# Kernel optimization log

Hardware: AMD Instinct MI355X
Metric: run time of the kernel (lower is better)

The kernel has to match this reference:

```python
import jax, jax.numpy as jnp
import numpy as np

THETA = 100000.0

def _rope(x, pos, theta=THETA):
    # x: [..., H, S, d_k]; pos: [S] int
    d_k = x.shape[-1]
    half = d_k // 2
    inv_freq = theta ** (-(jnp.arange(half, dtype=jnp.float32) / half))  # theta^{-2i/d}
    ang = pos.astype(jnp.float32)[:, None] * inv_freq[None, :]  # [S, half]
    cos, sin = jnp.cos(ang), jnp.sin(ang)
    x1 = x[..., 0::2]
    x2 = x[..., 1::2]
    r1 = x1 * cos - x2 * sin
    r2 = x1 * sin + x2 * cos
    # interleave back to [..., d_k]
    return jnp.stack([r1, r2], axis=-1).reshape(x.shape)


def setup_inputs() -> dict:
    key = jax.random.key(0)
    ks = jax.random.split(key, 5)
    B, S, D = 1, 4096, 1024
    x = jax.random.normal(ks[0], (B, S, D), dtype=jnp.float32)
    sc = 1.0 / np.sqrt(D)
    Wq = jax.random.normal(ks[1], (D, D), dtype=jnp.float32) * sc
    Wk = jax.random.normal(ks[2], (D, D), dtype=jnp.float32) * sc
    Wv = jax.random.normal(ks[3], (D, D), dtype=jnp.float32) * sc
    Wo = jax.random.normal(ks[4], (D, D), dtype=jnp.float32) * sc
    token_positions = jnp.arange(S, dtype=jnp.int32)
    return {"x": x, "Wq": Wq, "Wk": Wk, "Wv": Wv, "Wo": Wo, "token_positions": token_positions}


def reference(x, Wq, Wk, Wv, Wo, token_positions):
    H = 16
    B, S, D = x.shape
    d_k = D // H
    # Linear (no bias): y = x @ W^T
    Q = jnp.einsum('bsd,ed->bse', x, Wq)
    K = jnp.einsum('bsd,ed->bse', x, Wk)
    V = jnp.einsum('bsd,ed->bse', x, Wv)
    # [B, H, S, d_k]
    Q = Q.reshape(B, S, H, d_k).transpose(0, 2, 1, 3)
    K = K.reshape(B, S, H, d_k).transpose(0, 2, 1, 3)
    V = V.reshape(B, S, H, d_k).transpose(0, 2, 1, 3)
    Q = _rope(Q, token_positions)
    K = _rope(K, token_positions)
    scores = jnp.einsum('bhqd,bhkd->bhqk', Q, K) / jnp.sqrt(jnp.float32(d_k))
    causal = jnp.tril(jnp.ones((S, S), dtype=bool))
    scores = jnp.where(causal, scores, jnp.finfo(scores.dtype).min)
    probs = jax.nn.softmax(scores, axis=-1)
    attn = jnp.einsum('bhqk,bhkd->bhqd', probs, V)
    attn = attn.transpose(0, 2, 1, 3).reshape(B, S, D)
    return jnp.einsum('bsd,ed->bse', attn, Wo)
```

## Files before the change

### kernel.cpp

```cpp
#include <hip/hip_runtime.h>

typedef float f32x4 __attribute__((ext_vector_type(4)));
typedef short s16x8 __attribute__((ext_vector_type(8)));
typedef int   i32x2 __attribute__((ext_vector_type(2)));
typedef int   i32x4 __attribute__((ext_vector_type(4)));

#define DEV static __device__ __forceinline__

DEV short f2bf(float f) {
    unsigned u = __builtin_bit_cast(unsigned, f);
    u += 0x7FFFu + ((u >> 16) & 1u);
    return (short)(u >> 16);
}
DEV float bf2f(short s) {
    return __builtin_bit_cast(float, ((unsigned)(unsigned short)s) << 16);
}
DEV int cvtpk(float lo, float hi) {
    int r;
    asm("v_cvt_pk_bf16_f32 %0, %1, %2" : "=v"(r) : "v"(lo), "v"(hi));
    return r;
}
DEV float fexp2(float x) { float r; asm("v_exp_f32 %0, %1" : "=v"(r) : "v"(x)); return r; }
DEV float ffract(float x){ float r; asm("v_fract_f32 %0, %1" : "=v"(r) : "v"(x)); return r; }
DEV float fsin(float x)  { float r; asm("v_sin_f32 %0, %1" : "=v"(r) : "v"(x)); return r; }
DEV float fcos(float x)  { float r; asm("v_cos_f32 %0, %1" : "=v"(r) : "v"(x)); return r; }
DEV f32x4 mfma_bf16(s16x8 a, s16x8 b, f32x4 c) {
    asm("v_mfma_f32_16x16x32_bf16 %0, %1, %2, %0" : "+v"(c) : "v"(a), "v"(b));
    return c;
}
DEV f32x4 mfma16_bf16(i32x2 a, i32x2 b, f32x4 c) {
    asm("v_mfma_f32_16x16x16_bf16 %0, %1, %2, %0" : "+v"(c) : "v"(a), "v"(b));
    return c;
}
DEV void gl_lds16(const void* g, void* l) {
    __builtin_amdgcn_global_load_lds((const __attribute__((address_space(1))) unsigned*)g,
                                     (__attribute__((address_space(3))) unsigned*)l, 16, 0, 0);
}

__global__ __launch_bounds__(256) void conv_kernel(
    const float* __restrict__ x,
    const float* __restrict__ W0, const float* __restrict__ W1,
    const float* __restrict__ W2, const float* __restrict__ W3,
    short* __restrict__ xb,
    short* __restrict__ B0, short* __restrict__ B1,
    short* __restrict__ B2, short* __restrict__ B3)
{
    const int bid = blockIdx.x, tid = threadIdx.x;
    const float* src;
    short* dst;
    size_t off;
    if (bid < 2048) {
        src = x; dst = xb; off = (size_t)bid * 2048 + tid * 8;
    } else {
        int t = bid - 2048, wi = t >> 9;
        src = wi == 0 ? W0 : (wi == 1 ? W1 : (wi == 2 ? W2 : W3));
        dst = wi == 0 ? B0 : (wi == 1 ? B1 : (wi == 2 ? B2 : B3));
        off = (size_t)(t & 511) * 2048 + tid * 8;
    }
    f32x4 v0 = *(const f32x4*)(src + off);
    f32x4 v1 = *(const f32x4*)(src + off + 4);
    s16x8 o;
    #pragma unroll
    for (int e = 0; e < 4; e++) { o[e] = f2bf(v0[e]); o[4 + e] = f2bf(v1[e]); }
    *(s16x8*)(dst + off) = o;
}

template<int BM, int OUT_BF16, int ROPE>
__global__ __launch_bounds__(256) void gemm128(
    const short* __restrict__ A,
    const short* __restrict__ Bq, const short* __restrict__ Bk, const short* __restrict__ Bv,
    void* __restrict__ Cq, void* __restrict__ Ck, void* __restrict__ Cv,
    const int* __restrict__ posp)
{
    constexpr int KD = 1024, ND = 1024;
    constexpr int MI = BM / 32;
    __shared__ __align__(16) short As[BM * 32];
    __shared__ __align__(16) short Bs[128 * 32];
    const int n0 = blockIdx.x * 128, m0 = blockIdx.y * BM;
    const int zz = blockIdx.z;
    const short* B = zz == 0 ? Bq : (zz == 1 ? Bk : Bv);
    void* C       = zz == 0 ? Cq : (zz == 1 ? Ck : Cv);
    const int tid = threadIdx.x;
    const int lane = tid & 63, w = tid >> 6, g = lane >> 4, c = lane & 15;
    const int wm = w >> 1, wn = w & 1;

    const int swz = (tid & 3) ^ ((tid >> 3) & 3);
    const short* a0 = A + (size_t)(m0 + (tid >> 2)) * KD + 8 * swz;
    const short* a1 = a0 + (size_t)64 * KD;
    const short* b0 = B + (size_t)(n0 + (tid >> 2)) * KD + 8 * swz;
    const short* b1 = b0 + (size_t)64 * KD;
    char* ldsA = (char*)As + w * 1024;
    char* ldsB = (char*)Bs + w * 1024;

    int aoff[MI], boff[4];
    #pragma unroll
    for (int i = 0; i < MI; i++) {
        int ar = wm * (BM / 2) + i * 16 + c;
        aoff[i] = ar * 64 + (g ^ ((ar >> 1) & 3)) * 16;
    }
    #pragma unroll
    for (int j = 0; j < 4; j++) {
        int br = wn * 64 + j * 16 + c;
        boff[j] = br * 64 + (g ^ ((br >> 1) & 3)) * 16;
    }

    f32x4 acc[MI][4] = {};

    for (int k0 = 0; k0 < KD; k0 += 32) {
        __syncthreads();
        gl_lds16(a0 + k0, ldsA);
        if (BM == 128) gl_lds16(a1 + k0, ldsA + 4096);
        gl_lds16(b0 + k0, ldsB);
        gl_lds16(b1 + k0, ldsB + 4096);
        __syncthreads();
        s16x8 af[MI], bf[4];
        #pragma unroll
        for (int i = 0; i < MI; i++) af[i] = *(const s16x8*)((const char*)As + aoff[i]);
        #pragma unroll
        for (int j = 0; j < 4; j++) bf[j] = *(const s16x8*)((const char*)Bs + boff[j]);
        #pragma unroll
        for (int i = 0; i < MI; i++)
            #pragma unroll
            for (int j = 0; j < 4; j++)
                acc[i][j] = mfma_bf16(af[i], bf[j], acc[i][j]);
    }

    if (ROPE && zz <= 1) {
        const float ps = (zz == 0) ? 0.18033688011112042f : 1.0f;
        #pragma unroll
        for (int j = 0; j < 4; j++) {
            int col = n0 + wn * 64 + j * 16 + c;
            float invf = fexp2(-(float)((col & 63) >> 1) * 0.51905126482615036f)
                       * 0.15915494309189535f;
            float ssign = (col & 1) ? 1.f : -1.f;
            #pragma unroll
            for (int i = 0; i < MI; i++)
                #pragma unroll
                for (int r = 0; r < 4; r++) {
                    int row = m0 + wm * (BM / 2) + i * 16 + 4 * g + r;
                    float fp = (float)posp[row];
                    float fr = ffract(fp * invf);
                    float sn = fsin(fr) * ps, cs = fcos(fr) * ps;
                    float own = acc[i][j][r];
                    float oth = __shfl_xor(own, 1);
                    acc[i][j][r] = own * cs + oth * (ssign * sn);
                }
        }
    }

    #pragma unroll
    for (int i = 0; i < MI; i++)
        #pragma unroll
        for (int j = 0; j < 4; j++)
            #pragma unroll
            for (int r = 0; r < 4; r++) {
                int row = m0 + wm * (BM / 2) + i * 16 + 4 * g + r;
                int col = n0 + wn * 64 + j * 16 + c;
                float v = acc[i][j][r];
                if (OUT_BF16) ((short*)C)[(size_t)row * ND + col] = f2bf(v);
                else          ((float*)C)[(size_t)row * ND + col] = v;
            }
}

template<int A_BF16, int OUT_BF16>
__global__ __launch_bounds__(256) void gemm_bt(
    const void* __restrict__ Ap,
    const float* __restrict__ B0, const float* __restrict__ B1, const float* __restrict__ B2,
    void* __restrict__ C0, void* __restrict__ C1, void* __restrict__ C2)
{
    constexpr int KD = 1024, ND = 1024;
    __shared__ short As[64][40];
    __shared__ short Bs[64][40];
    const int n0 = blockIdx.x * 64, m0 = blockIdx.y * 64;
    const float* Bw = blockIdx.z == 0 ? B0 : (blockIdx.z == 1 ? B1 : B2);
    void* Cw       = blockIdx.z == 0 ? C0 : (blockIdx.z == 1 ? C1 : C2);
    const int tid = threadIdx.x;
    const int lane = tid & 63, w = tid >> 6, g = lane >> 4, c = lane & 15;
    const int wm = w >> 1, wn = w & 1;
    const int sr = tid >> 2, scc = (tid & 3) * 8;

    f32x4 acc[2][2] = {};

    for (int k0 = 0; k0 < KD; k0 += 32) {
        __syncthreads();
        if (A_BF16) {
            *(s16x8*)&As[sr][scc] =
                *(const s16x8*)((const short*)Ap + (size_t)(m0 + sr) * KD + k0 + scc);
        } else {
            const float* ap = (const float*)Ap + (size_t)(m0 + sr) * KD + k0 + scc;
            f32x4 va = *(const f32x4*)ap, vb = *(const f32x4*)(ap + 4);
            s16x8 av;
            #pragma unroll
            for (int e = 0; e < 4; e++) { av[e] = f2bf(va[e]); av[4 + e] = f2bf(vb[e]); }
            *(s16x8*)&As[sr][scc] = av;
        }
        {
            const float* bp = Bw + (size_t)(n0 + sr) * KD + k0 + scc;
            f32x4 va = *(const f32x4*)bp, vb = *(const f32x4*)(bp + 4);
            s16x8 bv;
            #pragma unroll
            for (int e = 0; e < 4; e++) { bv[e] = f2bf(va[e]); bv[4 + e] = f2bf(vb[e]); }
            *(s16x8*)&Bs[sr][scc] = bv;
        }
        __syncthreads();
        s16x8 af[2], bfv[2];
        #pragma unroll
        for (int i = 0; i < 2; i++) af[i]  = *(const s16x8*)&As[wm * 32 + i * 16 + c][8 * g];
        #pragma unroll
        for (int j = 0; j < 2; j++) bfv[j] = *(const s16x8*)&Bs[wn * 32 + j * 16 + c][8 * g];
        #pragma unroll
        for (int i = 0; i < 2; i++)
            #pragma unroll
            for (int j = 0; j < 2; j++)
                acc[i][j] = mfma_bf16(af[i], bfv[j], acc[i][j]);
    }

    #pragma unroll
    for (int i = 0; i < 2; i++)
        #pragma unroll
        for (int j = 0; j < 2; j++)
            #pragma unroll
            for (int r = 0; r < 4; r++) {
                int row = m0 + wm * 32 + i * 16 + 4 * g + r;
                int col = n0 + wn * 32 + j * 16 + c;
                float v = acc[i][j][r];
                if (OUT_BF16) ((short*)Cw)[(size_t)row * ND + col] = f2bf(v);
                else          ((float*)Cw)[(size_t)row * ND + col] = v;
            }
}

__global__ __launch_bounds__(256) void rope_kernel(short* Q, short* K, const int* __restrict__ posp)
{
    const int t = blockIdx.x * 256 + threadIdx.x;
    const int isK = blockIdx.y;
    short* ptr = isK ? K : Q;
    const float postscale = isK ? 1.0f : 0.18033688011112042f;
    const int idx  = t * 8;
    const int srow = idx >> 10;
    const int dd   = (idx & 1023) & 63;
    const int p0   = dd >> 1;
    const float fp = (float)posp[srow];
    s16x8 v = *(s16x8*)(ptr + idx);
    s16x8 o;
    #pragma unroll
    for (int pr = 0; pr < 4; pr++) {
        float ex  = fexp2(-(float)(p0 + pr) * 0.51905126482615036f);
        float ang = fp * ex * 0.15915494309189535f;
        float fr  = ffract(ang);
        float sn  = fsin(fr) * postscale;
        float cs  = fcos(fr) * postscale;
        float x1 = bf2f(v[2 * pr]), x2 = bf2f(v[2 * pr + 1]);
        o[2 * pr]     = f2bf(x1 * cs - x2 * sn);
        o[2 * pr + 1] = f2bf(x1 * sn + x2 * cs);
    }
    *(s16x8*)(ptr + idx) = o;
}

template<int SPLIT>
__global__ __launch_bounds__(512, 2) void attn_kernel(
    const short* __restrict__ Q, const short* __restrict__ K,
    const short* __restrict__ V, short* __restrict__ O0,
    short* __restrict__ O1, float* __restrict__ Lf)
{
    constexpr int D = 1024;
    constexpr int ST = 1 + SPLIT;
    int qx, h, z;
    if (SPLIT) {
        const int B = blockIdx.x;
        const int xcd = B & 7, k = B >> 3;
        h = xcd + 8 * (k >> 5);
        const int r = k & 31;
        qx = r & 15;
        z = r >> 4;
    } else {
        qx = blockIdx.x; h = blockIdx.y; z = 0;
    }
    const int hc = h * 64;
    short* O = (SPLIT && z) ? O1 : O0;
    const int tid = threadIdx.x;
    const int w = tid >> 6, lane = tid & 63, g = lane >> 4, c = lane & 15;

    __shared__ __align__(16) int Kl[2][64 * 32];
    __shared__ __align__(16) int Vl[2][64][32];

    const int wk = w & 3;
    const int krow_l = lane >> 3;
    const int kchunk = (lane & 7) ^ krow_l;
    const short* Kpre = K + hc + (size_t)(wk * 16 + krow_l) * D + kchunk * 8;
    char* kdst0 = (char*)&Kl[0][0] + wk * 16 * 128;
    char* kdst1 = (char*)&Kl[1][0] + wk * 16 * 128;

    const int vtid = tid & 255;
    const int vkvp = vtid & 31;
    const int vd0 = (vtid >> 5) * 8;
    const short* Vpre = V + hc + (size_t)(2 * vkvp) * D + vd0;

    int koff0[4], koff1[4];
    #pragma unroll
    for (int t = 0; t < 4; t++) {
        int row = t * 16 + c;
        koff0[t] = row * 128 + ((g) ^ (row & 7)) * 16;
        koff1[t] = row * 128 + ((4 + g) ^ (row & 7)) * 16;
    }

    for (int pi = 0; pi < 2; pi++) {
        const int qq = pi ? 31 - qx : qx;
        const int wq_min = qq * 128 + w * 16;
        const int qrow = wq_min + c;
        const short* qp = Q + (size_t)qrow * D + hc + 8 * g;
        const s16x8 bq0 = *(const s16x8*)qp;
        const s16x8 bq1 = *(const s16x8*)(qp + 32);

        f32x4 acc[4] = {};
        float l = 0.f;
        const int nkb = 2 * qq + 2;

        __syncthreads();
        s16x8 vs0, vs1;
        {
            if (w < 4) {
                gl_lds16(Kpre + (size_t)(z * 64) * D, kdst0);
                gl_lds16(Kpre + (size_t)(z * 64 + 8) * D, kdst0 + 8 * 128);
            } else {
                const short* vp = Vpre + (size_t)(z * 64) * D;
                vs0 = *(const s16x8*)vp;
                vs1 = *(const s16x8*)(vp + D);
            }
        }

        int cur = 0;
        for (int kb = z; kb < nkb; kb += ST, cur ^= 1) {
            if (w >= 4) {
                #pragma unroll
                for (int e = 0; e < 8; e++) {
                    unsigned dw = (unsigned)(unsigned short)vs0[e] | ((unsigned)(unsigned short)vs1[e] << 16);
                    Vl[cur][vd0 + e][vkvp ^ (4 * e)] = (int)dw;
                }
            }
            asm volatile("s_waitcnt vmcnt(0)" ::: "memory");
            __syncthreads();

            const bool more = (kb + ST) < nkb;
            if (more) {
                const int kb1 = kb + ST;
                if (w < 4) {
                    char* kd = cur ? kdst0 : kdst1;
                    gl_lds16(Kpre + (size_t)(kb1 * 64) * D, kd);
                    gl_lds16(Kpre + (size_t)(kb1 * 64 + 8) * D, kd + 8 * 128);
                } else {
                    const short* vp = Vpre + (size_t)(kb1 * 64) * D;
                    vs0 = *(const s16x8*)vp;
                    vs1 = *(const s16x8*)(vp + D);
                }
            }

            if (kb * 64 > wq_min + 15) continue;

            const char* Kb = (const char*)&Kl[cur][0];
            f32x4 st[4];
            __builtin_amdgcn_s_setprio(1);
            #pragma unroll
            for (int t = 0; t < 4; t++) {
                s16x8 a0 = *(const s16x8*)(Kb + koff0[t]);
                s16x8 a1 = *(const s16x8*)(Kb + koff1[t]);
                f32x4 zf = {};
                zf = mfma_bf16(a0, bq0, zf);
                zf = mfma_bf16(a1, bq1, zf);
                st[t] = zf;
            }
            __builtin_amdgcn_s_setprio(0);

            float p[16];
            if (kb * 64 + 63 > wq_min) {
                #pragma unroll
                for (int t = 0; t < 4; t++)
                    #pragma unroll
                    for (int i = 0; i < 4; i++) {
                        int kv = kb * 64 + t * 16 + 4 * g + i;
                        float e = fexp2(st[t][i]);
                        if (kv > qrow) e = 0.f;
                        p[t * 4 + i] = e;
                        l += e;
                    }
            } else {
                #pragma unroll
                for (int t = 0; t < 4; t++)
                    #pragma unroll
                    for (int i = 0; i < 4; i++) {
                        float e = fexp2(st[t][i]);
                        p[t * 4 + i] = e;
                        l += e;
                    }
            }

            i32x2 pd[4];
            #pragma unroll
            for (int t = 0; t < 4; t++) {
                pd[t][0] = cvtpk(p[t * 4 + 0], p[t * 4 + 1]);
                pd[t][1] = cvtpk(p[t * 4 + 2], p[t * 4 + 3]);
            }

            __builtin_amdgcn_s_setprio(1);
            #pragma unroll
            for (int t = 0; t < 4; t++) {
                #pragma unroll
                for (int jt = 0; jt < 4; jt++) {
                    i32x2 vb = *(const i32x2*)&Vl[cur][jt * 16 + c][(t * 8 + 2 * g) ^ (4 * (c & 7))];
                    acc[jt] = mfma16_bf16(pd[t], vb, acc[jt]);
                }
            }
            __builtin_amdgcn_s_setprio(0);
        }

        float lsum = l + __shfl_xor(l, 16);
        lsum += __shfl_xor(lsum, 32);
        if (SPLIT && lane < 16) {
            float Lv = (lsum > 0.f) ? __log2f(lsum) : -1e30f;
            Lf[(size_t)(z * 16 + h) * 4096 + (qq * 128 + w * 16 + lane)] = Lv;
        }
        float linv[4];
        #pragma unroll
        for (int i = 0; i < 4; i++) {
            float ls = __shfl(lsum, 4 * g + i);
            linv[i] = (ls > 0.f) ? 1.f / ls : 0.f;
        }
        #pragma unroll
        for (int jt = 0; jt < 4; jt++)
            #pragma unroll
            for (int i = 0; i < 4; i++) {
                int r = qq * 128 + w * 16 + 4 * g + i;
                O[(size_t)r * D + hc + jt * 16 + c] = f2bf(acc[jt][i] * linv[i]);
            }
    }
}

__global__ __launch_bounds__(256) void combine_kernel(
    short* __restrict__ Aw, const short* __restrict__ P1, const float* __restrict__ Lf)
{
    const int t = blockIdx.x * 256 + threadIdx.x;
    const int idx = t * 8;
    const int row = idx >> 10, col = idx & 1023, h = col >> 6;
    float L0 = Lf[(size_t)h * 4096 + row];
    float L1 = Lf[(size_t)(16 + h) * 4096 + row];
    float LM = fmaxf(L0, L1);
    float w0 = fexp2(L0 - LM), w1 = fexp2(L1 - LM);
    float inv = 1.f / (w0 + w1);
    w0 *= inv; w1 *= inv;
    s16x8 a = *(s16x8*)(Aw + idx);
    s16x8 b = *(const s16x8*)(P1 + idx);
    s16x8 o;
    #pragma unroll
    for (int e = 0; e < 8; e++)
        o[e] = f2bf(w0 * bf2f(a[e]) + w1 * bf2f(b[e]));
    *(s16x8*)(Aw + idx) = o;
}

extern "C" void kernel_launch(void* const* d_in, const int* in_sizes, int n_in,
                              void* d_out, int out_size, void* d_ws, size_t ws_size,
                              hipStream_t stream)
{
    const float* x  = (const float*)d_in[0];
    const float* Wq = (const float*)d_in[1];
    const float* Wk = (const float*)d_in[2];
    const float* Wv = (const float*)d_in[3];
    const float* Wo = (const float*)d_in[4];
    const int*  pos = (const int*)d_in[5];
    float* out = (float*)d_out;

    const size_t SD = (size_t)4096 * 1024;
    const size_t WSZ = (size_t)1024 * 1024;
    short* Qw = (short*)d_ws;
    short* Kw = Qw + SD;
    short* Vw = Kw + SD;
    short* Aw = Vw + SD;

    const size_t need_A = (5 * SD + 4 * WSZ) * sizeof(short) + 2 * 16 * 4096 * sizeof(float);
    const size_t need_B = (4 * SD + 4 * WSZ) * sizeof(short);

    if (ws_size >= need_A) {
        short* P1  = Aw + SD;
        short* xb  = Aw;
        short* Wqb = P1 + SD;
        short* Wkb = Wqb + WSZ;
        short* Wvb = Wkb + WSZ;
        short* Wob = Wvb + WSZ;
        float* Lf  = (float*)(Wob + WSZ);
        conv_kernel<<<4096, 256, 0, stream>>>(x, Wq, Wk, Wv, Wo, xb, Wqb, Wkb, Wvb, Wob);
        gemm128<128, 1, 1><<<dim3(8, 32, 3), 256, 0, stream>>>(xb, Wqb, Wkb, Wvb, Qw, Kw, Vw, pos);
        attn_kernel<1><<<512, 512, 0, stream>>>(Qw, Kw, Vw, Aw, P1, Lf);
        combine_kernel<<<2048, 256, 0, stream>>>(Aw, P1, Lf);
        gemm128<64, 0, 0><<<dim3(8, 64, 1), 256, 0, stream>>>(Aw, Wob, Wob, Wob, out, out, out, pos);
    } else if (ws_size >= need_B) {
        short* xb  = Aw;
        short* Wqb = Aw + SD;
        short* Wkb = Wqb + WSZ;
        short* Wvb = Wkb + WSZ;
        short* Wob = Wvb + WSZ;
        conv_kernel<<<4096, 256, 0, stream>>>(x, Wq, Wk, Wv, Wo, xb, Wqb, Wkb, Wvb, Wob);
        gemm128<128, 1, 1><<<dim3(8, 32, 3), 256, 0, stream>>>(xb, Wqb, Wkb, Wvb, Qw, Kw, Vw, pos);
        attn_kernel<0><<<dim3(16, 16, 1), 512, 0, stream>>>(Qw, Kw, Vw, Aw, Aw, nullptr);
        gemm128<64, 0, 0><<<dim3(8, 64, 1), 256, 0, stream>>>(Aw, Wob, Wob, Wob, out, out, out, pos);
    } else {
        gemm_bt<0, 1><<<dim3(16, 64, 3), 256, 0, stream>>>(x, Wq, Wk, Wv, Qw, Kw, Vw);
        rope_kernel<<<dim3(2048, 2), 256, 0, stream>>>(Qw, Kw, pos);
        attn_kernel<0><<<dim3(16, 16, 1), 512, 0, stream>>>(Qw, Kw, Vw, Aw, Aw, nullptr);
        gemm_bt<1, 0><<<dim3(16, 64, 1), 256, 0, stream>>>(Aw, Wo, Wo, Wo, out, out, out);
    }
}
```

Before: 131.2 us.

## Split attention KV range four ways with generalized log-sum-exp combine

Generalizes the split-KV attention kernel from two to NZ partitions and launches a 4-way split (1024 blocks) when the workspace is large enough. The combine kernel merges NP partial outputs using per-row log2 sums. The aim is more parallelism to fill CUs and balance the causal workload. In exchange, it adds extra partial-output writes and reads, and raises the launch bound occupancy hint, which may force register limits or spills.

```diff
diff --git a/kernel.cpp b/kernel.cpp
--- a/kernel.cpp
+++ b/kernel.cpp
@@ -256,27 +256,27 @@
     *(s16x8*)(ptr + idx) = o;
 }
 
-template<int SPLIT>
-__global__ __launch_bounds__(512, 2) void attn_kernel(
+template<int NZ>
+__global__ __launch_bounds__(512, 8) void attn_kernel(
     const short* __restrict__ Q, const short* __restrict__ K,
     const short* __restrict__ V, short* __restrict__ O0,
-    short* __restrict__ O1, float* __restrict__ Lf)
+    short* __restrict__ O1, short* __restrict__ O2, short* __restrict__ O3,
+    float* __restrict__ Lf)
 {
     constexpr int D = 1024;
-    constexpr int ST = 1 + SPLIT;
     int qx, h, z;
-    if (SPLIT) {
+    if (NZ > 1) {
         const int B = blockIdx.x;
         const int xcd = B & 7, k = B >> 3;
-        h = xcd + 8 * (k >> 5);
-        const int r = k & 31;
+        h = xcd + 8 * (k / (16 * NZ));
+        const int r = k % (16 * NZ);
         qx = r & 15;
         z = r >> 4;
     } else {
         qx = blockIdx.x; h = blockIdx.y; z = 0;
     }
     const int hc = h * 64;
-    short* O = (SPLIT && z) ? O1 : O0;
+    short* O = (z == 0) ? O0 : (z == 1 ? O1 : (z == 2 ? O2 : O3));
     const int tid = threadIdx.x;
     const int w = tid >> 6, lane = tid & 63, g = lane >> 4, c = lane & 15;
 
@@ -329,7 +329,7 @@
         }
 
         int cur = 0;
-        for (int kb = z; kb < nkb; kb += ST, cur ^= 1) {
+        for (int kb = z; kb < nkb; kb += NZ, cur ^= 1) {
             if (w >= 4) {
                 #pragma unroll
                 for (int e = 0; e < 8; e++) {
@@ -340,9 +340,9 @@
             asm volatile("s_waitcnt vmcnt(0)" ::: "memory");
             __syncthreads();
 
-            const bool more = (kb + ST) < nkb;
+            const bool more = (kb + NZ) < nkb;
             if (more) {
-                const int kb1 = kb + ST;
+                const int kb1 = kb + NZ;
                 if (w < 4) {
                     char* kd = cur ? kdst0 : kdst1;
                     gl_lds16(Kpre + (size_t)(kb1 * 64) * D, kd);
@@ -414,7 +414,7 @@
 
         float lsum = l + __shfl_xor(l, 16);
         lsum += __shfl_xor(lsum, 32);
-        if (SPLIT && lane < 16) {
+        if (NZ > 1 && lane < 16) {
             float Lv = (lsum > 0.f) ? __log2f(lsum) : -1e30f;
             Lf[(size_t)(z * 16 + h) * 4096 + (qq * 128 + w * 16 + lane)] = Lv;
         }
@@ -434,24 +434,42 @@
     }
 }
 
+template<int NP>
 __global__ __launch_bounds__(256) void combine_kernel(
-    short* __restrict__ Aw, const short* __restrict__ P1, const float* __restrict__ Lf)
+    short* __restrict__ Aw, const short* __restrict__ P1,
+    const short* __restrict__ P2, const short* __restrict__ P3,
+    const float* __restrict__ Lf)
 {
     const int t = blockIdx.x * 256 + threadIdx.x;
     const int idx = t * 8;
     const int row = idx >> 10, col = idx & 1023, h = col >> 6;
-    float L0 = Lf[(size_t)h * 4096 + row];
-    float L1 = Lf[(size_t)(16 + h) * 4096 + row];
-    float LM = fmaxf(L0, L1);
-    float w0 = fexp2(L0 - LM), w1 = fexp2(L1 - LM);
-    float inv = 1.f / (w0 + w1);
-    w0 *= inv; w1 *= inv;
-    s16x8 a = *(s16x8*)(Aw + idx);
-    s16x8 b = *(const s16x8*)(P1 + idx);
+    float L[NP];
+    float LM = -1e30f;
+    #pragma unroll
+    for (int zi = 0; zi < NP; zi++) {
+        L[zi] = Lf[(size_t)(zi * 16 + h) * 4096 + row];
+        LM = fmaxf(LM, L[zi]);
+    }
+    float wz[NP], wsum = 0.f;
+    #pragma unroll
+    for (int zi = 0; zi < NP; zi++) { wz[zi] = fexp2(L[zi] - LM); wsum += wz[zi]; }
+    float inv = 1.f / wsum;
+    #pragma unroll
+    for (int zi = 0; zi < NP; zi++) wz[zi] *= inv;
+
+    const short* Ps[4] = {Aw, P1, P2, P3};
+    f32x4 o0 = {}, o1 = {};
+    #pragma unroll
+    for (int zi = 0; zi < NP; zi++) {
+        s16x8 a = *(const s16x8*)(Ps[zi] + idx);
+        #pragma unroll
+        for (int e = 0; e < 4; e++) o0[e] += wz[zi] * bf2f(a[e]);
+        #pragma unroll
+        for (int e = 0; e < 4; e++) o1[e] += wz[zi] * bf2f(a[4 + e]);
+    }
     s16x8 o;
     #pragma unroll
-    for (int e = 0; e < 8; e++)
-        o[e] = f2bf(w0 * bf2f(a[e]) + w1 * bf2f(b[e]));
+    for (int e = 0; e < 4; e++) { o[e] = f2bf(o0[e]); o[4 + e] = f2bf(o1[e]); }
     *(s16x8*)(Aw + idx) = o;
 }
 
@@ -474,10 +492,26 @@
     short* Vw = Kw + SD;
     short* Aw = Vw + SD;
 
-    const size_t need_A = (5 * SD + 4 * WSZ) * sizeof(short) + 2 * 16 * 4096 * sizeof(float);
-    const size_t need_B = (4 * SD + 4 * WSZ) * sizeof(short);
-
-    if (ws_size >= need_A) {
+    const size_t need_A4 = (7 * SD + 4 * WSZ) * sizeof(short) + 4 * 16 * 4096 * sizeof(float);
+    const size_t need_A2 = (5 * SD + 4 * WSZ) * sizeof(short) + 2 * 16 * 4096 * sizeof(float);
+    const size_t need_B  = (4 * SD + 4 * WSZ) * sizeof(short);
+
+    if (ws_size >= need_A4) {
+        short* P1  = Aw + SD;
+        short* P2  = P1 + SD;
+        short* P3  = P2 + SD;
+        short* xb  = Aw;
+        short* Wqb = P3 + SD;
+        short* Wkb = Wqb + WSZ;
+        short* Wvb = Wkb + WSZ;
+        short* Wob = Wvb + WSZ;
+        float* Lf  = (float*)(Wob + WSZ);
+        conv_kernel<<<4096, 256, 0, stream>>>(x, Wq, Wk, Wv, Wo, xb, Wqb, Wkb, Wvb, Wob);
+        gemm128<128, 1, 1><<<dim3(8, 32, 3), 256, 0, stream>>>(xb, Wqb, Wkb, Wvb, Qw, Kw, Vw, pos);
+        attn_kernel<4><<<1024, 512, 0, stream>>>(Qw, Kw, Vw, Aw, P1, P2, P3, Lf);
+        combine_kernel<4><<<2048, 256, 0, stream>>>(Aw, P1, P2, P3, Lf);
+        gemm128<64, 0, 0><<<dim3(8, 64, 1), 256, 0, stream>>>(Aw, Wob, Wob, Wob, out, out, out, pos);
+    } else if (ws_size >= need_A2) {
         short* P1  = Aw + SD;
         short* xb  = Aw;
         short* Wqb = P1 + SD;
@@ -487,8 +521,8 @@
         float* Lf  = (float*)(Wob + WSZ);
         conv_kernel<<<4096, 256, 0, stream>>>(x, Wq, Wk, Wv, Wo, xb, Wqb, Wkb, Wvb, Wob);
         gemm128<128, 1, 1><<<dim3(8, 32, 3), 256, 0, stream>>>(xb, Wqb, Wkb, Wvb, Qw, Kw, Vw, pos);
-        attn_kernel<1><<<512, 512, 0, stream>>>(Qw, Kw, Vw, Aw, P1, Lf);
-        combine_kernel<<<2048, 256, 0, stream>>>(Aw, P1, Lf);
+        attn_kernel<2><<<512, 512, 0, stream>>>(Qw, Kw, Vw, Aw, P1, P1, P1, Lf);
+        combine_kernel<2><<<2048, 256, 0, stream>>>(Aw, P1, P1, P1, Lf);
         gemm128<64, 0, 0><<<dim3(8, 64, 1), 256, 0, stream>>>(Aw, Wob, Wob, Wob, out, out, out, pos);
     } else if (ws_size >= need_B) {
         short* xb  = Aw;
@@ -498,12 +532,12 @@
         short* Wob = Wvb + WSZ;
         conv_kernel<<<4096, 256, 0, stream>>>(x, Wq, Wk, Wv, Wo, xb, Wqb, Wkb, Wvb, Wob);
         gemm128<128, 1, 1><<<dim3(8, 32, 3), 256, 0, stream>>>(xb, Wqb, Wkb, Wvb, Qw, Kw, Vw, pos);
-        attn_kernel<0><<<dim3(16, 16, 1), 512, 0, stream>>>(Qw, Kw, Vw, Aw, Aw, nullptr);
+        attn_kernel<1><<<dim3(16, 16, 1), 512, 0, stream>>>(Qw, Kw, Vw, Aw, Aw, Aw, Aw, nullptr);
         gemm128<64, 0, 0><<<dim3(8, 64, 1), 256, 0, stream>>>(Aw, Wob, Wob, Wob, out, out, out, pos);
     } else {
         gemm_bt<0, 1><<<dim3(16, 64, 3), 256, 0, stream>>>(x, Wq, Wk, Wv, Qw, Kw, Vw);
         rope_kernel<<<dim3(2048, 2), 256, 0, stream>>>(Qw, Kw, pos);
-        attn_kernel<0><<<dim3(16, 16, 1), 512, 0, stream>>>(Qw, Kw, Vw, Aw, Aw, nullptr);
+        attn_kernel<1><<<dim3(16, 16, 1), 512, 0, stream>>>(Qw, Kw, Vw, Aw, Aw, Aw, Aw, nullptr);
         gemm_bt<1, 0><<<dim3(16, 64, 1), 256, 0, stream>>>(Aw, Wo, Wo, Wo, out, out, out);
     }
 }
```

After: 210.8 us. 1.61x slower.
